# Optimization experiments

Hardware: AMD Instinct MI355X
Metric: run time of the kernel (lower is better)

## Reference

```python
import jax, jax.numpy as jnp
import numpy as np

N, F, O, K = 4096, 128, 128, 4


def setup_inputs() -> dict:
    key = jax.random.key(0)
    ks = jax.random.split(key, 7)
    shift = jax.random.uniform(ks[0], (N, N), jnp.float32) * (1.0 / N)  # dense stand-in for sparse adjacency
    A2 = shift * shift  # elementwise square, as in torch.mul(all_A, all_A)
    x = jax.random.normal(ks[1], (N, F), jnp.float32)
    nan_mask = jax.random.bernoulli(ks[2], 0.1, (N, F))
    features = jnp.where(nan_mask, jnp.nan, x)
    limit = float(np.sqrt(6.0 / (F + O)))  # xavier_uniform
    weight = jax.random.uniform(ks[3], (F, O), jnp.float32, -limit, limit)
    pi = jnp.log(jax.nn.softmax(jax.random.normal(ks[4], (K,), jnp.float32)))  # log mixture weights
    mu = jax.random.normal(ks[5], (K, F), jnp.float32)  # GMM means
    sigma = jnp.log(jax.random.uniform(ks[6], (K, F), jnp.float32, minval=0.5, maxval=1.5))  # log diag covs
    return {"shift": shift, "features": features, "weight": weight,
            "pi": pi, "mu": mu, "sigma": sigma, "A2": A2}


def ex_relu(mu_t, sig_t):
    # E[relu(X)] for X ~ N(mu_t, sig_t), with exact relu fallback when variance == 0
    is_zero = sig_t == 0
    s = jnp.where(is_zero, 1e-10, sig_t)
    sqrt_s = jnp.sqrt(s)
    w = mu_t / sqrt_s
    inv_sqrt_2pi = 1.0 / np.sqrt(2.0 * np.pi)
    nr = sqrt_s * (jnp.exp(-0.5 * w * w) * inv_sqrt_2pi
                   + 0.5 * w * (1.0 + jax.lax.erf(w / np.sqrt(2.0))))
    return jnp.where(is_zero, jnp.maximum(mu_t, 0.0), nr)


def reference(shift, features, weight, pi, mu, sigma, A2):
    dim = features.shape[1]
    x_isnan = jnp.isnan(features)[None, :, :]            # [1, N, F] -> broadcasts over K
    variances = jnp.exp(sigma)                           # [K, F]
    # GMM imputation: mean/variance per component where features missing
    mean_mat = jnp.where(x_isnan, mu[:, None, :], features[None, :, :])      # [K, N, F]
    var_mat = jnp.where(x_isnan, variances[:, None, :], 0.0)                 # [K, N, F]
    # dense GEMMs
    transform_x = jnp.einsum('knf,fo->kno', mean_mat, weight)                # [K, N, O]
    transform_covs = jnp.einsum('knf,fo->kno', var_mat, weight * weight)     # [K, N, O]
    # K graph propagations (spmm in the original)
    conv_x = jnp.einsum('nm,kmo->kno', shift, transform_x)
    conv_covs = jnp.einsum('nm,kmo->kno', A2, transform_covs)
    expected_x = ex_relu(conv_x, conv_covs)                                  # [K, N, O]
    # responsibilities gamma: softmax over components of log pi + log N(x; mu, var)
    log_n = (-0.5 * jnp.sum((mean_mat - mu[:, None, :]) ** 2 / variances[:, None, :], axis=2)
             - 0.5 * dim * np.log(2.0 * np.pi) - 0.5 * jnp.sum(sigma))       # [K, N]
    gamma = jax.nn.softmax(pi[:, None] + log_n, axis=0)                      # [K, N]
    return jnp.sum(expected_x * gamma[:, :, None], axis=0)                   # [N, O]
```

## Files before the change

### kernel.cpp

```cpp
#include <hip/hip_runtime.h>


#define NN 4096
#define FF 128
#define KK 4

typedef _Float16 f16;
typedef f16 f16x8 __attribute__((ext_vector_type(8)));
typedef f16 f16x4 __attribute__((ext_vector_type(4)));
typedef float f32x4 __attribute__((ext_vector_type(4)));

typedef const __attribute__((address_space(1))) void* gptr1_t;
typedef __attribute__((address_space(3))) void* lptr3_t;

__device__ __forceinline__ void gload_lds16(const void* g, void* l) {
  __builtin_amdgcn_global_load_lds((gptr1_t)g, (lptr3_t)l, 16, 0, 0);
}

__device__ __forceinline__ bool is_nan_bits(float x) {
  return (__float_as_uint(x) & 0x7fffffffu) > 0x7f800000u;
}

__global__ __launch_bounds__(256) void k0_prep(
    const float* __restrict__ W, const float* __restrict__ mu,
    const float* __restrict__ sigma, f16* __restrict__ Wx, f16* __restrict__ Wc,
    f16* __restrict__ muh, f16* __restrict__ varh, float* __restrict__ invvar) {
  int tid = blockIdx.x * 256 + threadIdx.x;
  for (int i = tid; i < 16384; i += (int)gridDim.x * 256) {
    int j = i & 7;
    int o = (i >> 3) & 127;
    int g = (i >> 10) & 3;
    int fc = i >> 12;
    int f = fc * 32 + g * 8 + j;
    float w = W[f * 128 + o];
    Wx[i] = (f16)w;
    Wc[i] = (f16)(w * w);
  }
  if (tid < 512) {
    muh[tid] = (f16)mu[tid];
    float s = sigma[tid];
    varh[tid] = (f16)expf(s);
    invvar[tid] = expf(-s);
  }
}

__global__ __launch_bounds__(256) void kpre_shift(const float* __restrict__ shift,
                                                  f16* __restrict__ sh16) {
  long i = ((long)blockIdx.x * 256 + threadIdx.x) * 8;
  f32x4 a = *(const f32x4*)(shift + i);
  f32x4 b = *(const f32x4*)(shift + i + 4);
  f16x8 o;
#pragma unroll
  for (int j = 0; j < 4; ++j) o[j] = (f16)(a[j] * 4096.f);
#pragma unroll
  for (int j = 0; j < 4; ++j) o[4 + j] = (f16)(b[j] * 4096.f);
  *(f16x8*)(sh16 + i) = o;
}

__global__ __launch_bounds__(256) void k1a_gamma(
    const float* __restrict__ feats, const float* __restrict__ mu,
    const float* __restrict__ pi, const float* __restrict__ invvar,
    float* __restrict__ gamma) {
  int wid = threadIdx.x >> 6, lane = threadIdx.x & 63;
  int n = blockIdx.x * 4 + wid;
  const float* rp = feats + (long)n * FF;
  float x0 = rp[lane], x1 = rp[lane + 64];
  bool nan0 = is_nan_bits(x0), nan1 = is_nan_bits(x1);
  float acc[KK];
#pragma unroll
  for (int k = 0; k < KK; ++k) {
    float d0 = x0 - mu[k * FF + lane];
    float d1 = x1 - mu[k * FF + lane + 64];
    float t0 = nan0 ? 0.f : d0 * d0 * invvar[k * FF + lane];
    float t1 = nan1 ? 0.f : d1 * d1 * invvar[k * FF + lane + 64];
    acc[k] = t0 + t1;
  }
#pragma unroll
  for (int off = 32; off > 0; off >>= 1) {
#pragma unroll
    for (int k = 0; k < KK; ++k) acc[k] += __shfl_down(acc[k], off);
  }
  if (lane == 0) {
    float lg[KK], m = -1e30f;
#pragma unroll
    for (int k = 0; k < KK; ++k) {
      lg[k] = pi[k] - 0.5f * acc[k];
      m = fmaxf(m, lg[k]);
    }
    float e[KK], s = 0.f;
#pragma unroll
    for (int k = 0; k < KK; ++k) {
      e[k] = expf(lg[k] - m);
      s += e[k];
    }
    float inv = 1.f / s;
#pragma unroll
    for (int k = 0; k < KK; ++k) gamma[k * NN + n] = e[k] * inv;
  }
}

__global__ __launch_bounds__(256, 2) void k1b_transform(
    const float* __restrict__ feats, const f16* __restrict__ Wx,
    const f16* __restrict__ Wc, const f16* __restrict__ muh,
    const f16* __restrict__ varh, f16* __restrict__ Bws) {
  __shared__ __align__(16) f16 lds[2][4][4][128][8];
  int bid = blockIdx.x;
  int row = bid & 31;
  int kc = bid >> 5;
  int n0 = row * 128;
  int tid = threadIdx.x;
  int wid = tid >> 6, lane = tid & 63;
  int wr = wid >> 1, wc = wid & 1;
  int fr = lane & 15, fg = lane >> 4;
  int sn = tid >> 1, sh = tid & 1;

  f32x4 accx[4][4], accc[4][4];
#pragma unroll
  for (int a = 0; a < 4; ++a)
#pragma unroll
    for (int b = 0; b < 4; ++b) {
      accx[a][b] = f32x4{0.f, 0.f, 0.f, 0.f};
      accc[a][b] = f32x4{0.f, 0.f, 0.f, 0.f};
    }

  const int NT = 4;
  float xs[16];
  f16 mh[16], vh[16];

  auto loadA = [&](int t) {
    const float* ap = feats + (long)(n0 + sn) * FF + t * 32 + sh * 16;
    *(f32x4*)(xs + 0) = *(const f32x4*)(ap + 0);
    *(f32x4*)(xs + 4) = *(const f32x4*)(ap + 4);
    *(f32x4*)(xs + 8) = *(const f32x4*)(ap + 8);
    *(f32x4*)(xs + 12) = *(const f32x4*)(ap + 12);
    const f16* mp = muh + kc * FF + t * 32 + sh * 16;
    const f16* vp = varh + kc * FF + t * 32 + sh * 16;
    *(f16x8*)(mh + 0) = *(const f16x8*)(mp + 0);
    *(f16x8*)(mh + 8) = *(const f16x8*)(mp + 8);
    *(f16x8*)(vh + 0) = *(const f16x8*)(vp + 0);
    *(f16x8*)(vh + 8) = *(const f16x8*)(vp + 8);
  };
  auto writeA = [&](int buf) {
    f16 am[16], av[16];
#pragma unroll
    for (int j = 0; j < 16; ++j) {
      float x = xs[j];
      bool nn = is_nan_bits(x);
      am[j] = nn ? mh[j] : (f16)x;
      av[j] = nn ? vh[j] : (f16)0.f;
    }
    *(f16x8*)&lds[buf][0][2 * sh + 0][sn][0] = *(f16x8*)(am + 0);
    *(f16x8*)&lds[buf][0][2 * sh + 1][sn][0] = *(f16x8*)(am + 8);
    *(f16x8*)&lds[buf][1][2 * sh + 0][sn][0] = *(f16x8*)(av + 0);
    *(f16x8*)&lds[buf][1][2 * sh + 1][sn][0] = *(f16x8*)(av + 8);
  };
  auto stageB = [&](int t, int buf) {
#pragma unroll
    for (int r = 0; r < 2; ++r) {
      int c = r * 256 + tid;
      int cb = r * 256 + wid * 64;
      gload_lds16(Wx + (long)t * 4096 + (long)c * 8, (f16*)&lds[buf][2][0][0][0] + (long)cb * 8);
      gload_lds16(Wc + (long)t * 4096 + (long)c * 8, (f16*)&lds[buf][3][0][0][0] + (long)cb * 8);
    }
  };
  auto compute = [&](int buf) {
    f16x8 am[4], av[4], bx[4], bc[4];
#pragma unroll
    for (int mf = 0; mf < 4; ++mf) {
      am[mf] = *(f16x8*)&lds[buf][0][fg][wr * 64 + mf * 16 + fr][0];
      av[mf] = *(f16x8*)&lds[buf][1][fg][wr * 64 + mf * 16 + fr][0];
    }
#pragma unroll
    for (int nf = 0; nf < 4; ++nf) {
      bx[nf] = *(f16x8*)&lds[buf][2][fg][wc * 64 + nf * 16 + fr][0];
      bc[nf] = *(f16x8*)&lds[buf][3][fg][wc * 64 + nf * 16 + fr][0];
    }
#pragma unroll
    for (int mf = 0; mf < 4; ++mf)
#pragma unroll
      for (int nf = 0; nf < 4; ++nf) {
        accx[mf][nf] = __builtin_amdgcn_mfma_f32_16x16x32_f16(am[mf], bx[nf], accx[mf][nf], 0, 0, 0);
        accc[mf][nf] = __builtin_amdgcn_mfma_f32_16x16x32_f16(av[mf], bc[nf], accc[mf][nf], 0, 0, 0);
      }
  };

  stageB(0, 0);
  loadA(0);
  writeA(0);
  __syncthreads();
  for (int t = 0; t < NT; ++t) {
    int cur = t & 1, nxt = cur ^ 1;
    if (t + 1 < NT) {
      stageB(t + 1, nxt);
      loadA(t + 1);
    }
    compute(cur);
    if (t + 1 < NT) writeA(nxt);
    __syncthreads();
  }

#pragma unroll
  for (int mf = 0; mf < 4; ++mf) {
    int nbase = n0 + wr * 64 + mf * 16 + fg * 4;
#pragma unroll
    for (int nf = 0; nf < 4; ++nf) {
      int col = wc * 64 + nf * 16 + fr;
      f16x4 px, pc;
#pragma unroll
      for (int j = 0; j < 4; ++j) {
        px[j] = (f16)accx[mf][nf][j];
        pc[j] = (f16)accc[mf][nf][j];
      }
      *(f16x4*)(Bws + (long)(kc * 128 + col) * NN + nbase) = px;
      *(f16x4*)(Bws + (long)(512 + kc * 128 + col) * NN + nbase) = pc;
    }
  }
}

__global__ __launch_bounds__(256, 4) void k2_conv(
    const f16* __restrict__ sh16, const f16* __restrict__ Bws,
    float* __restrict__ convbuf, int mlen) {
  __shared__ __align__(16) f16 la[2][4][128][8];
  __shared__ __align__(16) f16 lb[2][4][128][8];
  int bid = blockIdx.x;
  int ct = bid & 7;
  int row = (bid >> 3) & 31;
  int ks = bid >> 8;
  int n0 = row * 128;
  int col0 = ct * 128;
  bool cov = ct >= 4;
  int m0 = ks * mlen;
  int nt = mlen / 32;
  int tid = threadIdx.x;
  int wid = tid >> 6, lane = tid & 63;
  int wr = wid >> 1, wc = wid & 1;
  int fr = lane & 15, fg = lane >> 4;

  f32x4 acc[4][4];
#pragma unroll
  for (int a = 0; a < 4; ++a)
#pragma unroll
    for (int b = 0; b < 4; ++b) acc[a][b] = f32x4{0.f, 0.f, 0.f, 0.f};

  auto stage = [&](int t, int buf) {
#pragma unroll
    for (int r = 0; r < 2; ++r) {
      int c = r * 256 + tid;
      int idx = c & 127, g = c >> 7;
      int cb = r * 256 + wid * 64;
      gload_lds16(sh16 + (long)(n0 + idx) * NN + m0 + t * 32 + g * 8,
                  (f16*)&la[buf][0][0][0] + (long)cb * 8);
      gload_lds16(Bws + (long)(col0 + idx) * NN + m0 + t * 32 + g * 8,
                  (f16*)&lb[buf][0][0][0] + (long)cb * 8);
    }
  };
  auto compute = [&](int buf) {
    f16x8 af[4], bf[4];
#pragma unroll
    for (int mf = 0; mf < 4; ++mf)
      af[mf] = *(f16x8*)&la[buf][fg][wr * 64 + mf * 16 + fr][0];
#pragma unroll
    for (int nf = 0; nf < 4; ++nf)
      bf[nf] = *(f16x8*)&lb[buf][fg][wc * 64 + nf * 16 + fr][0];
    if (cov) {
#pragma unroll
      for (int mf = 0; mf < 4; ++mf) af[mf] = af[mf] * af[mf];
    }
#pragma unroll
    for (int mf = 0; mf < 4; ++mf)
#pragma unroll
      for (int nf = 0; nf < 4; ++nf)
        acc[mf][nf] = __builtin_amdgcn_mfma_f32_16x16x32_f16(af[mf], bf[nf], acc[mf][nf], 0, 0, 0);
  };

  stage(0, 0);
  __syncthreads();
  for (int t = 0; t < nt; ++t) {
    int cur = t & 1, nxt = cur ^ 1;
    if (t + 1 < nt) stage(t + 1, nxt);
    compute(cur);
    __syncthreads();
  }

  const float dsc = cov ? (1.f / 16777216.f) : (1.f / 4096.f);
  float* base = convbuf + ((long)ks * NN + n0) * 1024 + col0;
#pragma unroll
  for (int mf = 0; mf < 4; ++mf) {
#pragma unroll
    for (int nf = 0; nf < 4; ++nf) {
      int o = wc * 64 + nf * 16 + fr;
#pragma unroll
      for (int j = 0; j < 4; ++j) {
        int n = wr * 64 + mf * 16 + fg * 4 + j;
        base[(long)n * 1024 + o] = acc[mf][nf][j] * dsc;
      }
    }
  }
}

__global__ __launch_bounds__(256) void k3_out(
    const float* __restrict__ convbuf, const float* __restrict__ gamma,
    float* __restrict__ out, int nks) {
  int gid = blockIdx.x * 256 + threadIdx.x;
  int n = gid >> 7, o = gid & 127;
  float cx[KK], cc[KK];
#pragma unroll
  for (int k = 0; k < KK; ++k) {
    cx[k] = 0.f;
    cc[k] = 0.f;
  }
  for (int s = 0; s < nks; ++s) {
    const float* bp = convbuf + ((long)s * NN + n) * 1024;
#pragma unroll
    for (int k = 0; k < KK; ++k) {
      cx[k] += bp[k * 128 + o];
      cc[k] += bp[512 + k * 128 + o];
    }
  }
  const float inv_sqrt_2pi = 0.3989422804014327f;
  float r = 0.f;
#pragma unroll
  for (int k = 0; k < KK; ++k) {
    float s = cc[k];
    bool iz = (s == 0.f);
    float ss = iz ? 1e-10f : s;
    float sq = sqrtf(ss);
    float w = cx[k] / sq;
    float nr = sq * (expf(-0.5f * w * w) * inv_sqrt_2pi +
                     0.5f * w * (1.f + erff(w * 0.7071067811865476f)));
    float ex = iz ? fmaxf(cx[k], 0.f) : nr;
    r += ex * gamma[k * NN + n];
  }
  out[gid] = r;
}

extern "C" void kernel_launch(void* const* d_in, const int* in_sizes, int n_in,
                              void* d_out, int out_size, void* d_ws, size_t ws_size,
                              hipStream_t stream) {
  const float* shift = (const float*)d_in[0];
  const float* feats = (const float*)d_in[1];
  const float* W = (const float*)d_in[2];
  const float* pi = (const float*)d_in[3];
  const float* mu = (const float*)d_in[4];
  const float* sigma = (const float*)d_in[5];
  float* out = (float*)d_out;

  char* w = (char*)d_ws;
  f16* Wx = (f16*)w;        w += 16384 * 2;
  f16* Wc = (f16*)w;        w += 16384 * 2;
  f16* muh = (f16*)w;       w += 512 * 2;
  f16* varh = (f16*)w;      w += 512 * 2;
  float* invvar = (float*)w; w += 512 * 4;
  float* gamma = (float*)w; w += (size_t)KK * NN * 4;
  f16* Bws = (f16*)w;       w += (size_t)1024 * NN * 2;
  f16* sh16 = (f16*)w;      w += (size_t)NN * NN * 2;
  float* convbuf = (float*)w;
  size_t used = (size_t)(w - (char*)d_ws);
  size_t slab = (size_t)NN * 1024 * 4;
  int nks = 1;
  if (ws_size >= used + 4 * slab) nks = 4;
  else if (ws_size >= used + 2 * slab) nks = 2;

  hipLaunchKernelGGL(k0_prep, dim3(64), dim3(256), 0, stream, W, mu, sigma, Wx, Wc,
                     muh, varh, invvar);
  hipLaunchKernelGGL(kpre_shift, dim3((NN * (long)NN) / (256 * 8)), dim3(256), 0,
                     stream, shift, sh16);
  hipLaunchKernelGGL(k1a_gamma, dim3(NN / 4), dim3(256), 0, stream, feats, mu, pi,
                     invvar, gamma);
  hipLaunchKernelGGL(k1b_transform, dim3(4 * 32), dim3(256), 0, stream, feats, Wx, Wc,
                     muh, varh, Bws);
  hipLaunchKernelGGL(k2_conv, dim3(nks * 32 * 8), dim3(256), 0, stream, sh16, Bws,
                     convbuf, NN / nks);
  hipLaunchKernelGGL(k3_out, dim3(NN * 128 / 256), dim3(256), 0, stream, convbuf,
                     gamma, out, nks);
}
```

Baseline: 260.5 us.

## Replace split-K conv GEMM with 64-row tiles over full reduction

```diff
diff --git a/kernel.cpp b/kernel.cpp
--- a/kernel.cpp
+++ b/kernel.cpp
@@ -217,57 +217,60 @@
   }
 }
 
-__global__ __launch_bounds__(256, 4) void k2_conv(
+__global__ __launch_bounds__(256) void k2_conv(
     const f16* __restrict__ sh16, const f16* __restrict__ Bws,
-    float* __restrict__ convbuf, int mlen) {
-  __shared__ __align__(16) f16 la[2][4][128][8];
+    float* __restrict__ convbuf) {
+  __shared__ __align__(16) f16 la[2][4][64][8];
   __shared__ __align__(16) f16 lb[2][4][128][8];
   int bid = blockIdx.x;
   int ct = bid & 7;
-  int row = (bid >> 3) & 31;
-  int ks = bid >> 8;
-  int n0 = row * 128;
+  int row = bid >> 3;
+  int n0 = row * 64;
   int col0 = ct * 128;
   bool cov = ct >= 4;
-  int m0 = ks * mlen;
-  int nt = mlen / 32;
+  const int nt = NN / 32;
   int tid = threadIdx.x;
   int wid = tid >> 6, lane = tid & 63;
   int wr = wid >> 1, wc = wid & 1;
   int fr = lane & 15, fg = lane >> 4;
 
-  f32x4 acc[4][4];
-#pragma unroll
-  for (int a = 0; a < 4; ++a)
+  f32x4 acc[2][4];
+#pragma unroll
+  for (int a = 0; a < 2; ++a)
 #pragma unroll
     for (int b = 0; b < 4; ++b) acc[a][b] = f32x4{0.f, 0.f, 0.f, 0.f};
 
   auto stage = [&](int t, int buf) {
+    {
+      int c = tid;
+      int idx = c & 63, g = c >> 6;
+      int cb = wid * 64;
+      gload_lds16(sh16 + (long)(n0 + idx) * NN + t * 32 + g * 8,
+                  (f16*)&la[buf][0][0][0] + (long)cb * 8);
+    }
 #pragma unroll
     for (int r = 0; r < 2; ++r) {
       int c = r * 256 + tid;
       int idx = c & 127, g = c >> 7;
       int cb = r * 256 + wid * 64;
-      gload_lds16(sh16 + (long)(n0 + idx) * NN + m0 + t * 32 + g * 8,
-                  (f16*)&la[buf][0][0][0] + (long)cb * 8);
-      gload_lds16(Bws + (long)(col0 + idx) * NN + m0 + t * 32 + g * 8,
+      gload_lds16(Bws + (long)(col0 + idx) * NN + t * 32 + g * 8,
                   (f16*)&lb[buf][0][0][0] + (long)cb * 8);
     }
   };
   auto compute = [&](int buf) {
-    f16x8 af[4], bf[4];
-#pragma unroll
-    for (int mf = 0; mf < 4; ++mf)
-      af[mf] = *(f16x8*)&la[buf][fg][wr * 64 + mf * 16 + fr][0];
+    f16x8 af[2], bf[4];
+#pragma unroll
+    for (int mf = 0; mf < 2; ++mf)
+      af[mf] = *(f16x8*)&la[buf][fg][wr * 32 + mf * 16 + fr][0];
 #pragma unroll
     for (int nf = 0; nf < 4; ++nf)
       bf[nf] = *(f16x8*)&lb[buf][fg][wc * 64 + nf * 16 + fr][0];
     if (cov) {
 #pragma unroll
-      for (int mf = 0; mf < 4; ++mf) af[mf] = af[mf] * af[mf];
-    }
-#pragma unroll
-    for (int mf = 0; mf < 4; ++mf)
+      for (int mf = 0; mf < 2; ++mf) af[mf] = af[mf] * af[mf];
+    }
+#pragma unroll
+    for (int mf = 0; mf < 2; ++mf)
 #pragma unroll
       for (int nf = 0; nf < 4; ++nf)
         acc[mf][nf] = __builtin_amdgcn_mfma_f32_16x16x32_f16(af[mf], bf[nf], acc[mf][nf], 0, 0, 0);
@@ -283,15 +286,15 @@
   }
 
   const float dsc = cov ? (1.f / 16777216.f) : (1.f / 4096.f);
-  float* base = convbuf + ((long)ks * NN + n0) * 1024 + col0;
-#pragma unroll
-  for (int mf = 0; mf < 4; ++mf) {
+  float* base = convbuf + (long)n0 * 1024 + col0;
+#pragma unroll
+  for (int mf = 0; mf < 2; ++mf) {
 #pragma unroll
     for (int nf = 0; nf < 4; ++nf) {
       int o = wc * 64 + nf * 16 + fr;
 #pragma unroll
       for (int j = 0; j < 4; ++j) {
-        int n = wr * 64 + mf * 16 + fg * 4 + j;
+        int n = wr * 32 + mf * 16 + fg * 4 + j;
         base[(long)n * 1024 + o] = acc[mf][nf][j] * dsc;
       }
     }
@@ -300,35 +303,23 @@
 
 __global__ __launch_bounds__(256) void k3_out(
     const float* __restrict__ convbuf, const float* __restrict__ gamma,
-    float* __restrict__ out, int nks) {
+    float* __restrict__ out) {
   int gid = blockIdx.x * 256 + threadIdx.x;
   int n = gid >> 7, o = gid & 127;
-  float cx[KK], cc[KK];
-#pragma unroll
-  for (int k = 0; k < KK; ++k) {
-    cx[k] = 0.f;
-    cc[k] = 0.f;
-  }
-  for (int s = 0; s < nks; ++s) {
-    const float* bp = convbuf + ((long)s * NN + n) * 1024;
-#pragma unroll
-    for (int k = 0; k < KK; ++k) {
-      cx[k] += bp[k * 128 + o];
-      cc[k] += bp[512 + k * 128 + o];
-    }
-  }
+  const float* bp = convbuf + (long)n * 1024;
   const float inv_sqrt_2pi = 0.3989422804014327f;
   float r = 0.f;
 #pragma unroll
   for (int k = 0; k < KK; ++k) {
-    float s = cc[k];
+    float cx = bp[k * 128 + o];
+    float s = bp[512 + k * 128 + o];
     bool iz = (s == 0.f);
     float ss = iz ? 1e-10f : s;
     float sq = sqrtf(ss);
-    float w = cx[k] / sq;
+    float w = cx / sq;
     float nr = sq * (expf(-0.5f * w * w) * inv_sqrt_2pi +
                      0.5f * w * (1.f + erff(w * 0.7071067811865476f)));
-    float ex = iz ? fmaxf(cx[k], 0.f) : nr;
+    float ex = iz ? fmaxf(cx, 0.f) : nr;
     r += ex * gamma[k * NN + n];
   }
   out[gid] = r;
@@ -355,11 +346,6 @@
   f16* Bws = (f16*)w;       w += (size_t)1024 * NN * 2;
   f16* sh16 = (f16*)w;      w += (size_t)NN * NN * 2;
   float* convbuf = (float*)w;
-  size_t used = (size_t)(w - (char*)d_ws);
-  size_t slab = (size_t)NN * 1024 * 4;
-  int nks = 1;
-  if (ws_size >= used + 4 * slab) nks = 4;
-  else if (ws_size >= used + 2 * slab) nks = 2;
 
   hipLaunchKernelGGL(k0_prep, dim3(64), dim3(256), 0, stream, W, mu, sigma, Wx, Wc,
                      muh, varh, invvar);
@@ -369,8 +355,7 @@
                      invvar, gamma);
   hipLaunchKernelGGL(k1b_transform, dim3(4 * 32), dim3(256), 0, stream, feats, Wx, Wc,
                      muh, varh, Bws);
-  hipLaunchKernelGGL(k2_conv, dim3(nks * 32 * 8), dim3(256), 0, stream, sh16, Bws,
-                     convbuf, NN / nks);
+  hipLaunchKernelGGL(k2_conv, dim3(64 * 8), dim3(256), 0, stream, sh16, Bws, convbuf);
   hipLaunchKernelGGL(k3_out, dim3(NN * 128 / 256), dim3(256), 0, stream, convbuf,
-                     gamma, out, nks);
-}
+                     gamma, out);
+}
```

Result: slower. 268.5 us (+3.1%).
